# Optimization experiments

Hardware: AMD Instinct MI355X
Metric: run time of the kernel (lower is better)

Reference implementation:

```python
import jax, jax.numpy as jnp
import numpy as np

N, D, E, T, K = 65536, 512, 256, 128, 5
ALPHA = 0.8  # residual_alpha


def _ln(x, gamma, beta, eps=1e-6):
    mu = jnp.mean(x, axis=-1, keepdims=True)
    var = jnp.mean(jnp.square(x - mu), axis=-1, keepdims=True)
    return (x - mu) * jax.lax.rsqrt(var + eps) * gamma + beta


def _normalize(x, eps=1e-6):
    n = jnp.linalg.norm(x, axis=-1, keepdims=True)
    return x / jnp.maximum(n, eps)


def setup_inputs() -> dict:
    key = jax.random.key(0)
    ks = jax.random.split(key, 8)
    return {
        "raw_memory": jax.random.normal(ks[0], (N, D), dtype=jnp.float32),
        "node_features": jax.random.normal(ks[1], (N, E), dtype=jnp.float32),
        "edge_features": jax.random.normal(ks[2], (N, E), dtype=jnp.float32),
        "time_encoding": jax.random.normal(ks[3], (N, T), dtype=jnp.float32),
        "prototypes": jax.random.normal(ks[4], (N, K, D), dtype=jnp.float32),
        "Wq": jax.random.normal(ks[5], (D, D + E + T), dtype=jnp.float32) * 0.02,
        "bq": jnp.zeros((D,), dtype=jnp.float32),
        "Wg": jax.random.normal(ks[6], (1, 2 * D + T), dtype=jnp.float32) * 0.02,
        "bg": jnp.zeros((1,), dtype=jnp.float32),
        "gamma": jnp.ones((D,), dtype=jnp.float32),
        "beta": jnp.zeros((D,), dtype=jnp.float32),
        "temperature": jnp.ones((1,), dtype=jnp.float32),
    }


def reference(raw_memory, node_features, edge_features, time_encoding, prototypes,
              Wq, bq, Wg, bg, gamma, beta, temperature):
    # _sanitize_tensor on finite inputs == clamp (nan_to_num is a no-op)
    raw = jnp.clip(raw_memory, -50.0, 50.0)
    edge_q = jnp.clip(edge_features, -50.0, 50.0)
    time_q = jnp.clip(time_encoding, -50.0, 50.0)

    # query projection (SpectralLinear in eval mode == plain linear) + shared LN + tanh
    q_in = jnp.concatenate([raw, edge_q, time_q], axis=-1)      # [N, D+E+T]
    query = jnp.tanh(_ln(q_in @ Wq.T + bq, gamma, beta))        # [N, D]

    # cosine similarity against per-node prototypes
    q_s = jnp.clip(query, -20.0, 20.0)
    p_s = jnp.clip(prototypes, -20.0, 20.0)
    sim = jnp.einsum('nd,nkd->nk', _normalize(q_s), _normalize(p_s))  # [N, K]
    sim = jnp.clip(sim, -15.0, 15.0)
    temp = jnp.clip(temperature, 0.5, 5.0)
    sim = sim / (temp + 1e-4)

    attn = jnp.clip(jax.nn.softmax(sim, axis=-1), 0.0, 1.0)    # dropout inactive (eval)

    cand = jnp.einsum('nk,nkd->nd', attn, prototypes)           # [N, D]
    cand = jnp.clip(cand, -5.0, 5.0)

    # gate (note: uses raw, un-sanitized time_encoding, then clamps)
    gate_cat = jnp.clip(jnp.concatenate([raw, cand, time_encoding], axis=-1), -30.0, 30.0)
    gate_logits = jnp.clip(gate_cat @ Wg.T + bg, -10.0, 10.0)   # [N, 1]
    g = jax.nn.sigmoid(gate_logits)

    gated = (1.0 - g) * raw + g * cand
    updated = ALPHA * raw + (1.0 - ALPHA) * gated
    updated = jnp.clip(_ln(updated, gamma, beta), -10.0, 10.0)  # final clamp(-50,50) is a no-op
    return updated
```

## Files before the change

kernel.cpp:

```cpp
#include <hip/hip_runtime.h>

#define NROWS 65536
#define DDIM  512
#define EDIM  256
#define TDIM  128
#define KTOT  896
#define MT    32
#define APAD  904

using bf16x8 = __attribute__((ext_vector_type(8))) short;
using f32x4  = __attribute__((ext_vector_type(4))) float;

static __device__ __forceinline__ unsigned short f2bf(float f) {
    unsigned int u = __float_as_uint(f);
    return (unsigned short)((u + 0x7fffu + ((u >> 16) & 1u)) >> 16);
}
static __device__ __forceinline__ float clampf(float x, float lo, float hi) {
    return fminf(fmaxf(x, lo), hi);
}
static __device__ __forceinline__ float wred_sum(float v) {
    #pragma unroll
    for (int m = 32; m > 0; m >>= 1) v += __shfl_xor(v, m, 64);
    return v;
}
static __device__ __forceinline__ float tanh_fast(float x) {
    x = clampf(x, -15.f, 15.f);
    float e = __expf(2.f * x);
    return (e - 1.f) / (e + 1.f);
}

__global__ void k_conv_wq(const float* __restrict__ wq, unsigned short* __restrict__ o) {
    int i = blockIdx.x * 256 + threadIdx.x;
    float4 v = ((const float4*)wq)[i];
    ushort4 r;
    r.x = f2bf(v.x); r.y = f2bf(v.y); r.z = f2bf(v.z); r.w = f2bf(v.w);
    ((ushort4*)o)[i] = r;
}

__global__ __launch_bounds__(256, 2) void k_qproj(
    const float* __restrict__ raw, const float* __restrict__ edge,
    const float* __restrict__ timee, const unsigned short* __restrict__ wqb,
    const float* __restrict__ bq, const float* __restrict__ gamma,
    const float* __restrict__ beta, float* __restrict__ qout)
{
    __shared__ union {
        unsigned short a[MT * APAD];
        float          c[MT * DDIM];
    } sm;

    const int tid = threadIdx.x;
    const int R0  = blockIdx.x * MT;

    #pragma unroll
    for (int i = 0; i < 16; ++i) {
        int idx = i * 256 + tid;
        int row = idx >> 7, c4 = idx & 127;
        float4 v = ((const float4*)(raw + (size_t)(R0 + row) * DDIM))[c4];
        unsigned int lo = (unsigned)f2bf(clampf(v.x, -50.f, 50.f)) |
                          ((unsigned)f2bf(clampf(v.y, -50.f, 50.f)) << 16);
        unsigned int hi = (unsigned)f2bf(clampf(v.z, -50.f, 50.f)) |
                          ((unsigned)f2bf(clampf(v.w, -50.f, 50.f)) << 16);
        *(uint2*)(&sm.a[row * APAD + c4 * 4]) = make_uint2(lo, hi);
    }
    #pragma unroll
    for (int i = 0; i < 8; ++i) {
        int idx = i * 256 + tid;
        int row = idx >> 6, c4 = idx & 63;
        float4 v = ((const float4*)(edge + (size_t)(R0 + row) * EDIM))[c4];
        unsigned int lo = (unsigned)f2bf(clampf(v.x, -50.f, 50.f)) |
                          ((unsigned)f2bf(clampf(v.y, -50.f, 50.f)) << 16);
        unsigned int hi = (unsigned)f2bf(clampf(v.z, -50.f, 50.f)) |
                          ((unsigned)f2bf(clampf(v.w, -50.f, 50.f)) << 16);
        *(uint2*)(&sm.a[row * APAD + DDIM + c4 * 4]) = make_uint2(lo, hi);
    }
    #pragma unroll
    for (int i = 0; i < 4; ++i) {
        int idx = i * 256 + tid;
        int row = idx >> 5, c4 = idx & 31;
        float4 v = ((const float4*)(timee + (size_t)(R0 + row) * TDIM))[c4];
        unsigned int lo = (unsigned)f2bf(clampf(v.x, -50.f, 50.f)) |
                          ((unsigned)f2bf(clampf(v.y, -50.f, 50.f)) << 16);
        unsigned int hi = (unsigned)f2bf(clampf(v.z, -50.f, 50.f)) |
                          ((unsigned)f2bf(clampf(v.w, -50.f, 50.f)) << 16);
        *(uint2*)(&sm.a[row * APAD + DDIM + EDIM + c4 * 4]) = make_uint2(lo, hi);
    }
    __syncthreads();

    const int w = tid >> 6, l = tid & 63, mlo = l & 15, quad = l >> 4;
    f32x4 acc[2][8];
    #pragma unroll
    for (int rt = 0; rt < 2; ++rt)
        #pragma unroll
        for (int c = 0; c < 8; ++c) { acc[rt][c] = (f32x4){0.f, 0.f, 0.f, 0.f}; }

    const unsigned short* bbase  = wqb + (size_t)(w * 128 + mlo) * KTOT + quad * 8;
    const unsigned short* abase0 = &sm.a[ mlo        * APAD + quad * 8];
    const unsigned short* abase1 = &sm.a[(16 + mlo)  * APAD + quad * 8];

    for (int k0 = 0; k0 < KTOT; k0 += 32) {
        bf16x8 a0 = *(const bf16x8*)(abase0 + k0);
        bf16x8 a1 = *(const bf16x8*)(abase1 + k0);
        #pragma unroll
        for (int c = 0; c < 8; ++c) {
            bf16x8 b = *(const bf16x8*)(bbase + (size_t)c * 16 * KTOT + k0);
            acc[0][c] = __builtin_amdgcn_mfma_f32_16x16x32_bf16(a0, b, acc[0][c], 0, 0, 0);
            acc[1][c] = __builtin_amdgcn_mfma_f32_16x16x32_bf16(a1, b, acc[1][c], 0, 0, 0);
        }
    }

    __syncthreads();
    #pragma unroll
    for (int rt = 0; rt < 2; ++rt)
        #pragma unroll
        for (int c = 0; c < 8; ++c)
            #pragma unroll
            for (int r = 0; r < 4; ++r)
                sm.c[(rt * 16 + quad * 4 + r) * DDIM + w * 128 + c * 16 + mlo] = acc[rt][c][r];
    __syncthreads();

    float bqv[8], gv[8], bv[8];
    #pragma unroll
    for (int j = 0; j < 8; ++j) {
        int d = l + 64 * j;
        bqv[j] = bq[d]; gv[j] = gamma[d]; bv[j] = beta[d];
    }
    for (int rr = 0; rr < 8; ++rr) {
        int r = w * 8 + rr;
        float v[8], s = 0.f, sq = 0.f;
        #pragma unroll
        for (int j = 0; j < 8; ++j) {
            v[j] = sm.c[r * DDIM + l + 64 * j] + bqv[j];
            s += v[j]; sq += v[j] * v[j];
        }
        s = wred_sum(s); sq = wred_sum(sq);
        float mu  = s * (1.f / 512.f);
        float var = sq * (1.f / 512.f) - mu * mu;
        float rs  = rsqrtf(fmaxf(var, 0.f) + 1e-6f);
        #pragma unroll
        for (int j = 0; j < 8; ++j) {
            float y = (v[j] - mu) * rs * gv[j] + bv[j];
            qout[(size_t)(R0 + r) * DDIM + l + 64 * j] = tanh_fast(y);
        }
    }
}

__global__ __launch_bounds__(256) void k_attn(
    const float* __restrict__ raw, const float* __restrict__ timee,
    const float* __restrict__ prot, const float* __restrict__ wg,
    const float* __restrict__ bg, const float* __restrict__ gamma,
    const float* __restrict__ beta, const float* __restrict__ temperature,
    float* __restrict__ out)
{
    const int R = blockIdx.x * 4 + (threadIdx.x >> 6);
    const int l = threadIdx.x & 63;
    const size_t rbase = (size_t)R * DDIM;

    float q[8], rw[8], p[5][8], tv[2];
    #pragma unroll
    for (int j = 0; j < 8; ++j) {
        q[j]  = out[rbase + l + 64 * j];
        rw[j] = clampf(raw[rbase + l + 64 * j], -50.f, 50.f);
    }
    tv[0] = timee[(size_t)R * TDIM + l];
    tv[1] = timee[(size_t)R * TDIM + l + 64];
    #pragma unroll
    for (int k = 0; k < 5; ++k)
        #pragma unroll
        for (int j = 0; j < 8; ++j)
            p[k][j] = prot[((size_t)R * 5 + k) * DDIM + l + 64 * j];

    float qs = 0.f;
    #pragma unroll
    for (int j = 0; j < 8; ++j) qs += q[j] * q[j];
    qs = wred_sum(qs);
    float qinv = 1.f / fmaxf(sqrtf(qs), 1e-6f);

    float sim[5];
    #pragma unroll
    for (int k = 0; k < 5; ++k) {
        float d = 0.f, pn = 0.f;
        #pragma unroll
        for (int j = 0; j < 8; ++j) {
            float ps = clampf(p[k][j], -20.f, 20.f);
            d += q[j] * ps; pn += ps * ps;
        }
        d = wred_sum(d); pn = wred_sum(pn);
        sim[k] = d * qinv * (1.f / fmaxf(sqrtf(pn), 1e-6f));
    }
    float temp = clampf(temperature[0], 0.5f, 5.f);
    float tinv = 1.f / (temp + 1e-4f);
    float mx = -1e30f;
    #pragma unroll
    for (int k = 0; k < 5; ++k) { sim[k] = clampf(sim[k], -15.f, 15.f) * tinv; mx = fmaxf(mx, sim[k]); }
    float e[5], Z = 0.f;
    #pragma unroll
    for (int k = 0; k < 5; ++k) { e[k] = __expf(sim[k] - mx); Z += e[k]; }
    float zi = 1.f / Z;
    #pragma unroll
    for (int k = 0; k < 5; ++k) e[k] = clampf(e[k] * zi, 0.f, 1.f);

    float cand[8];
    #pragma unroll
    for (int j = 0; j < 8; ++j) {
        float c = 0.f;
        #pragma unroll
        for (int k = 0; k < 5; ++k) c += e[k] * p[k][j];
        cand[j] = clampf(c, -5.f, 5.f);
    }

    float gp = 0.f;
    #pragma unroll
    for (int j = 0; j < 8; ++j) {
        int d = l + 64 * j;
        gp += wg[d]       * clampf(rw[j],   -30.f, 30.f);
        gp += wg[512 + d] * clampf(cand[j], -30.f, 30.f);
    }
    gp += wg[1024 + l]      * clampf(tv[0], -30.f, 30.f);
    gp += wg[1024 + l + 64] * clampf(tv[1], -30.f, 30.f);
    gp = wred_sum(gp);
    float gl = clampf(gp + bg[0], -10.f, 10.f);
    float g  = 1.f / (1.f + __expf(-gl));

    float u[8], s = 0.f, sq = 0.f;
    #pragma unroll
    for (int j = 0; j < 8; ++j) {
        float gated = (1.f - g) * rw[j] + g * cand[j];
        u[j] = 0.8f * rw[j] + 0.2f * gated;
        s += u[j]; sq += u[j] * u[j];
    }
    s = wred_sum(s); sq = wred_sum(sq);
    float mu  = s * (1.f / 512.f);
    float var = sq * (1.f / 512.f) - mu * mu;
    float rs  = rsqrtf(fmaxf(var, 0.f) + 1e-6f);
    #pragma unroll
    for (int j = 0; j < 8; ++j) {
        int d = l + 64 * j;
        float y = (u[j] - mu) * rs * gamma[d] + beta[d];
        out[rbase + d] = clampf(y, -10.f, 10.f);
    }
}

extern "C" void kernel_launch(void* const* d_in, const int* in_sizes, int n_in,
                              void* d_out, int out_size, void* d_ws, size_t ws_size,
                              hipStream_t stream) {
    const float* raw   = (const float*)d_in[0];
    const float* edge  = (const float*)d_in[2];
    const float* tim   = (const float*)d_in[3];
    const float* prot  = (const float*)d_in[4];
    const float* Wq    = (const float*)d_in[5];
    const float* bq    = (const float*)d_in[6];
    const float* Wg    = (const float*)d_in[7];
    const float* bg    = (const float*)d_in[8];
    const float* gamma = (const float*)d_in[9];
    const float* beta  = (const float*)d_in[10];
    const float* temp  = (const float*)d_in[11];
    float* out = (float*)d_out;
    unsigned short* wqb = (unsigned short*)d_ws;

    k_conv_wq<<<448, 256, 0, stream>>>(Wq, wqb);
    k_qproj<<<NROWS / MT, 256, 0, stream>>>(raw, edge, tim, wqb, bq, gamma, beta, out);
    k_attn <<<NROWS / 4, 256, 0, stream>>>(raw, tim, prot, Wg, bg, gamma, beta, temp, out);
}
```

Baseline: 1.335 ms.

## Fuse query projection with attention/gate epilogue and pre-swizzle Wq into MFMA fragment layout

Merges the query-projection kernel and the prototype attention/gating kernel into one, so the query is consumed from shared memory instead of being written to and re-read from global memory. The bf16 weight conversion now lays Wq out in MFMA B-fragment order, so each lane loads contiguous 16-byte chunks and all eight fragments are issued before the MFMAs. The epilogue switches to float4-vectorized loads and stores. In exchange, each block now does the long per-row attention epilogue serially after the GEMM, with more live registers, which may reduce overlap between the memory-bound and compute phases.

```diff
diff --git a/kernel.cpp b/kernel.cpp
--- a/kernel.cpp
+++ b/kernel.cpp
@@ -1,4 +1,5 @@
 #include <hip/hip_runtime.h>
+
 
 #define NROWS 65536
 #define DDIM  512
@@ -7,6 +8,7 @@
 #define KTOT  896
 #define MT    32
 #define APAD  904
+#define KS    28
 
 using bf16x8 = __attribute__((ext_vector_type(8))) short;
 using f32x4  = __attribute__((ext_vector_type(4))) float;
@@ -30,22 +32,30 @@
 }
 
 __global__ void k_conv_wq(const float* __restrict__ wq, unsigned short* __restrict__ o) {
-    int i = blockIdx.x * 256 + threadIdx.x;
-    float4 v = ((const float4*)wq)[i];
-    ushort4 r;
-    r.x = f2bf(v.x); r.y = f2bf(v.y); r.z = f2bf(v.z); r.w = f2bf(v.w);
-    ((ushort4*)o)[i] = r;
-}
-
-__global__ __launch_bounds__(256, 2) void k_qproj(
+    int t = blockIdx.x * 256 + threadIdx.x;
+    int l = t & 63, rest = t >> 6;
+    int ntile = rest & 31, ks = rest >> 5;
+    const float* src = wq + (size_t)(ntile * 16 + (l & 15)) * KTOT + ks * 32 + (l >> 4) * 8;
+    f32x4 v0 = ((const f32x4*)src)[0];
+    f32x4 v1 = ((const f32x4*)src)[1];
+    union { bf16x8 v; unsigned short u[8]; } r;
+    #pragma unroll
+    for (int j = 0; j < 4; ++j) { r.u[j] = f2bf(v0[j]); r.u[4 + j] = f2bf(v1[j]); }
+    ((bf16x8*)o)[t] = r.v;
+}
+
+__global__ __launch_bounds__(256, 2) void k_fused(
     const float* __restrict__ raw, const float* __restrict__ edge,
-    const float* __restrict__ timee, const unsigned short* __restrict__ wqb,
-    const float* __restrict__ bq, const float* __restrict__ gamma,
-    const float* __restrict__ beta, float* __restrict__ qout)
+    const float* __restrict__ timee, const unsigned short* __restrict__ wqs,
+    const float* __restrict__ bq, const float* __restrict__ wg,
+    const float* __restrict__ bg, const float* __restrict__ gamma,
+    const float* __restrict__ beta, const float* __restrict__ prot,
+    const float* __restrict__ temperature, float* __restrict__ out)
 {
     __shared__ union {
         unsigned short a[MT * APAD];
         float          c[MT * DDIM];
+        f32x4          c4[MT * DDIM / 4];
     } sm;
 
     const int tid = threadIdx.x;
@@ -54,35 +64,35 @@
     #pragma unroll
     for (int i = 0; i < 16; ++i) {
         int idx = i * 256 + tid;
-        int row = idx >> 7, c4 = idx & 127;
-        float4 v = ((const float4*)(raw + (size_t)(R0 + row) * DDIM))[c4];
+        int row = idx >> 7, c4i = idx & 127;
+        float4 v = ((const float4*)(raw + (size_t)(R0 + row) * DDIM))[c4i];
         unsigned int lo = (unsigned)f2bf(clampf(v.x, -50.f, 50.f)) |
                           ((unsigned)f2bf(clampf(v.y, -50.f, 50.f)) << 16);
         unsigned int hi = (unsigned)f2bf(clampf(v.z, -50.f, 50.f)) |
                           ((unsigned)f2bf(clampf(v.w, -50.f, 50.f)) << 16);
-        *(uint2*)(&sm.a[row * APAD + c4 * 4]) = make_uint2(lo, hi);
+        *(uint2*)(&sm.a[row * APAD + c4i * 4]) = make_uint2(lo, hi);
     }
     #pragma unroll
     for (int i = 0; i < 8; ++i) {
         int idx = i * 256 + tid;
-        int row = idx >> 6, c4 = idx & 63;
-        float4 v = ((const float4*)(edge + (size_t)(R0 + row) * EDIM))[c4];
+        int row = idx >> 6, c4i = idx & 63;
+        float4 v = ((const float4*)(edge + (size_t)(R0 + row) * EDIM))[c4i];
         unsigned int lo = (unsigned)f2bf(clampf(v.x, -50.f, 50.f)) |
                           ((unsigned)f2bf(clampf(v.y, -50.f, 50.f)) << 16);
         unsigned int hi = (unsigned)f2bf(clampf(v.z, -50.f, 50.f)) |
                           ((unsigned)f2bf(clampf(v.w, -50.f, 50.f)) << 16);
-        *(uint2*)(&sm.a[row * APAD + DDIM + c4 * 4]) = make_uint2(lo, hi);
+        *(uint2*)(&sm.a[row * APAD + DDIM + c4i * 4]) = make_uint2(lo, hi);
     }
     #pragma unroll
     for (int i = 0; i < 4; ++i) {
         int idx = i * 256 + tid;
-        int row = idx >> 5, c4 = idx & 31;
-        float4 v = ((const float4*)(timee + (size_t)(R0 + row) * TDIM))[c4];
+        int row = idx >> 5, c4i = idx & 31;
+        float4 v = ((const float4*)(timee + (size_t)(R0 + row) * TDIM))[c4i];
         unsigned int lo = (unsigned)f2bf(clampf(v.x, -50.f, 50.f)) |
                           ((unsigned)f2bf(clampf(v.y, -50.f, 50.f)) << 16);
         unsigned int hi = (unsigned)f2bf(clampf(v.z, -50.f, 50.f)) |
                           ((unsigned)f2bf(clampf(v.w, -50.f, 50.f)) << 16);
-        *(uint2*)(&sm.a[row * APAD + DDIM + EDIM + c4 * 4]) = make_uint2(lo, hi);
+        *(uint2*)(&sm.a[row * APAD + DDIM + EDIM + c4i * 4]) = make_uint2(lo, hi);
     }
     __syncthreads();
 
@@ -91,21 +101,24 @@
     #pragma unroll
     for (int rt = 0; rt < 2; ++rt)
         #pragma unroll
-        for (int c = 0; c < 8; ++c) { acc[rt][c] = (f32x4){0.f, 0.f, 0.f, 0.f}; }
-
-    const unsigned short* bbase  = wqb + (size_t)(w * 128 + mlo) * KTOT + quad * 8;
-    const unsigned short* abase0 = &sm.a[ mlo        * APAD + quad * 8];
-    const unsigned short* abase1 = &sm.a[(16 + mlo)  * APAD + quad * 8];
-
-    for (int k0 = 0; k0 < KTOT; k0 += 32) {
-        bf16x8 a0 = *(const bf16x8*)(abase0 + k0);
-        bf16x8 a1 = *(const bf16x8*)(abase1 + k0);
+        for (int c = 0; c < 8; ++c) acc[rt][c] = (f32x4){0.f, 0.f, 0.f, 0.f};
+
+    const unsigned short* abase0 = &sm.a[ mlo       * APAD + quad * 8];
+    const unsigned short* abase1 = &sm.a[(16 + mlo) * APAD + quad * 8];
+    const unsigned short* bptr   = wqs + ((size_t)(w * 8) * 64 + l) * 8;
+
+    for (int ks = 0; ks < KS; ++ks) {
+        bf16x8 a0 = *(const bf16x8*)(abase0 + ks * 32);
+        bf16x8 a1 = *(const bf16x8*)(abase1 + ks * 32);
+        bf16x8 bb[8];
+        #pragma unroll
+        for (int c = 0; c < 8; ++c) bb[c] = *(const bf16x8*)(bptr + c * 512);
         #pragma unroll
         for (int c = 0; c < 8; ++c) {
-            bf16x8 b = *(const bf16x8*)(bbase + (size_t)c * 16 * KTOT + k0);
-            acc[0][c] = __builtin_amdgcn_mfma_f32_16x16x32_bf16(a0, b, acc[0][c], 0, 0, 0);
-            acc[1][c] = __builtin_amdgcn_mfma_f32_16x16x32_bf16(a1, b, acc[1][c], 0, 0, 0);
-        }
+            acc[0][c] = __builtin_amdgcn_mfma_f32_16x16x32_bf16(a0, bb[c], acc[0][c], 0, 0, 0);
+            acc[1][c] = __builtin_amdgcn_mfma_f32_16x16x32_bf16(a1, bb[c], acc[1][c], 0, 0, 0);
+        }
+        bptr += 32 * 64 * 8;
     }
 
     __syncthreads();
@@ -114,129 +127,145 @@
         #pragma unroll
         for (int c = 0; c < 8; ++c)
             #pragma unroll
-            for (int r = 0; r < 4; ++r)
-                sm.c[(rt * 16 + quad * 4 + r) * DDIM + w * 128 + c * 16 + mlo] = acc[rt][c][r];
+            for (int r2 = 0; r2 < 4; ++r2)
+                sm.c[(rt * 16 + quad * 4 + r2) * DDIM + w * 128 + c * 16 + mlo] = acc[rt][c][r2];
     __syncthreads();
 
-    float bqv[8], gv[8], bv[8];
-    #pragma unroll
-    for (int j = 0; j < 8; ++j) {
-        int d = l + 64 * j;
-        bqv[j] = bq[d]; gv[j] = gamma[d]; bv[j] = beta[d];
-    }
+    f32x4 bq4[2], g4[2], b4[2], wgr4[2], wgc4[2];
+    #pragma unroll
+    for (int jj = 0; jj < 2; ++jj) {
+        bq4[jj]  = ((const f32x4*)bq)[l + 64 * jj];
+        g4[jj]   = ((const f32x4*)gamma)[l + 64 * jj];
+        b4[jj]   = ((const f32x4*)beta)[l + 64 * jj];
+        wgr4[jj] = ((const f32x4*)wg)[l + 64 * jj];
+        wgc4[jj] = ((const f32x4*)(wg + DDIM))[l + 64 * jj];
+    }
+    float wgt0 = wg[2 * DDIM + l], wgt1 = wg[2 * DDIM + l + 64];
+    float tmpv = clampf(temperature[0], 0.5f, 5.f);
+    float tinv = 1.f / (tmpv + 1e-4f);
+    float bgv  = bg[0];
+
     for (int rr = 0; rr < 8; ++rr) {
-        int r = w * 8 + rr;
-        float v[8], s = 0.f, sq = 0.f;
-        #pragma unroll
-        for (int j = 0; j < 8; ++j) {
-            v[j] = sm.c[r * DDIM + l + 64 * j] + bqv[j];
-            s += v[j]; sq += v[j] * v[j];
+        const int r = w * 8 + rr;
+        const size_t R = (size_t)(R0 + r);
+        const float* prow = prot + R * (5 * DDIM);
+
+        f32x4 p4[5][2];
+        #pragma unroll
+        for (int k = 0; k < 5; ++k) {
+            p4[k][0] = ((const f32x4*)(prow + k * DDIM))[l];
+            p4[k][1] = ((const f32x4*)(prow + k * DDIM))[l + 64];
+        }
+        f32x4 rw4[2];
+        #pragma unroll
+        for (int jj = 0; jj < 2; ++jj) {
+            f32x4 t = ((const f32x4*)(raw + R * DDIM))[l + 64 * jj];
+            #pragma unroll
+            for (int e2 = 0; e2 < 4; ++e2) rw4[jj][e2] = clampf(t[e2], -50.f, 50.f);
+        }
+        float t0 = timee[R * TDIM + l];
+        float t1 = timee[R * TDIM + l + 64];
+
+        f32x4 v4[2];
+        float s = 0.f, sq = 0.f;
+        #pragma unroll
+        for (int jj = 0; jj < 2; ++jj) {
+            f32x4 cv = sm.c4[r * 128 + l + 64 * jj];
+            cv += bq4[jj];
+            v4[jj] = cv;
+            #pragma unroll
+            for (int e2 = 0; e2 < 4; ++e2) { s += cv[e2]; sq += cv[e2] * cv[e2]; }
         }
         s = wred_sum(s); sq = wred_sum(sq);
         float mu  = s * (1.f / 512.f);
         float var = sq * (1.f / 512.f) - mu * mu;
         float rs  = rsqrtf(fmaxf(var, 0.f) + 1e-6f);
-        #pragma unroll
-        for (int j = 0; j < 8; ++j) {
-            float y = (v[j] - mu) * rs * gv[j] + bv[j];
-            qout[(size_t)(R0 + r) * DDIM + l + 64 * j] = tanh_fast(y);
-        }
-    }
-}
-
-__global__ __launch_bounds__(256) void k_attn(
-    const float* __restrict__ raw, const float* __restrict__ timee,
-    const float* __restrict__ prot, const float* __restrict__ wg,
-    const float* __restrict__ bg, const float* __restrict__ gamma,
-    const float* __restrict__ beta, const float* __restrict__ temperature,
-    float* __restrict__ out)
-{
-    const int R = blockIdx.x * 4 + (threadIdx.x >> 6);
-    const int l = threadIdx.x & 63;
-    const size_t rbase = (size_t)R * DDIM;
-
-    float q[8], rw[8], p[5][8], tv[2];
-    #pragma unroll
-    for (int j = 0; j < 8; ++j) {
-        q[j]  = out[rbase + l + 64 * j];
-        rw[j] = clampf(raw[rbase + l + 64 * j], -50.f, 50.f);
-    }
-    tv[0] = timee[(size_t)R * TDIM + l];
-    tv[1] = timee[(size_t)R * TDIM + l + 64];
-    #pragma unroll
-    for (int k = 0; k < 5; ++k)
-        #pragma unroll
-        for (int j = 0; j < 8; ++j)
-            p[k][j] = prot[((size_t)R * 5 + k) * DDIM + l + 64 * j];
-
-    float qs = 0.f;
-    #pragma unroll
-    for (int j = 0; j < 8; ++j) qs += q[j] * q[j];
-    qs = wred_sum(qs);
-    float qinv = 1.f / fmaxf(sqrtf(qs), 1e-6f);
-
-    float sim[5];
-    #pragma unroll
-    for (int k = 0; k < 5; ++k) {
-        float d = 0.f, pn = 0.f;
-        #pragma unroll
-        for (int j = 0; j < 8; ++j) {
-            float ps = clampf(p[k][j], -20.f, 20.f);
-            d += q[j] * ps; pn += ps * ps;
-        }
-        d = wred_sum(d); pn = wred_sum(pn);
-        sim[k] = d * qinv * (1.f / fmaxf(sqrtf(pn), 1e-6f));
-    }
-    float temp = clampf(temperature[0], 0.5f, 5.f);
-    float tinv = 1.f / (temp + 1e-4f);
-    float mx = -1e30f;
-    #pragma unroll
-    for (int k = 0; k < 5; ++k) { sim[k] = clampf(sim[k], -15.f, 15.f) * tinv; mx = fmaxf(mx, sim[k]); }
-    float e[5], Z = 0.f;
-    #pragma unroll
-    for (int k = 0; k < 5; ++k) { e[k] = __expf(sim[k] - mx); Z += e[k]; }
-    float zi = 1.f / Z;
-    #pragma unroll
-    for (int k = 0; k < 5; ++k) e[k] = clampf(e[k] * zi, 0.f, 1.f);
-
-    float cand[8];
-    #pragma unroll
-    for (int j = 0; j < 8; ++j) {
-        float c = 0.f;
-        #pragma unroll
-        for (int k = 0; k < 5; ++k) c += e[k] * p[k][j];
-        cand[j] = clampf(c, -5.f, 5.f);
-    }
-
-    float gp = 0.f;
-    #pragma unroll
-    for (int j = 0; j < 8; ++j) {
-        int d = l + 64 * j;
-        gp += wg[d]       * clampf(rw[j],   -30.f, 30.f);
-        gp += wg[512 + d] * clampf(cand[j], -30.f, 30.f);
-    }
-    gp += wg[1024 + l]      * clampf(tv[0], -30.f, 30.f);
-    gp += wg[1024 + l + 64] * clampf(tv[1], -30.f, 30.f);
-    gp = wred_sum(gp);
-    float gl = clampf(gp + bg[0], -10.f, 10.f);
-    float g  = 1.f / (1.f + __expf(-gl));
-
-    float u[8], s = 0.f, sq = 0.f;
-    #pragma unroll
-    for (int j = 0; j < 8; ++j) {
-        float gated = (1.f - g) * rw[j] + g * cand[j];
-        u[j] = 0.8f * rw[j] + 0.2f * gated;
-        s += u[j]; sq += u[j] * u[j];
-    }
-    s = wred_sum(s); sq = wred_sum(sq);
-    float mu  = s * (1.f / 512.f);
-    float var = sq * (1.f / 512.f) - mu * mu;
-    float rs  = rsqrtf(fmaxf(var, 0.f) + 1e-6f);
-    #pragma unroll
-    for (int j = 0; j < 8; ++j) {
-        int d = l + 64 * j;
-        float y = (u[j] - mu) * rs * gamma[d] + beta[d];
-        out[rbase + d] = clampf(y, -10.f, 10.f);
+        f32x4 q4[2];
+        float qs = 0.f;
+        #pragma unroll
+        for (int jj = 0; jj < 2; ++jj)
+            #pragma unroll
+            for (int e2 = 0; e2 < 4; ++e2) {
+                float y = (v4[jj][e2] - mu) * rs * g4[jj][e2] + b4[jj][e2];
+                y = tanh_fast(y);
+                q4[jj][e2] = y;
+                qs += y * y;
+            }
+        qs = wred_sum(qs);
+        float qinv = 1.f / fmaxf(sqrtf(qs), 1e-6f);
+
+        float sim[5];
+        #pragma unroll
+        for (int k = 0; k < 5; ++k) {
+            float d = 0.f, pn = 0.f;
+            #pragma unroll
+            for (int jj = 0; jj < 2; ++jj)
+                #pragma unroll
+                for (int e2 = 0; e2 < 4; ++e2) {
+                    float ps = clampf(p4[k][jj][e2], -20.f, 20.f);
+                    d  += q4[jj][e2] * ps;
+                    pn += ps * ps;
+                }
+            d = wred_sum(d); pn = wred_sum(pn);
+            sim[k] = d * qinv * (1.f / fmaxf(sqrtf(pn), 1e-6f));
+        }
+        float mx = -1e30f;
+        #pragma unroll
+        for (int k = 0; k < 5; ++k) { sim[k] = clampf(sim[k], -15.f, 15.f) * tinv; mx = fmaxf(mx, sim[k]); }
+        float ek[5], Z = 0.f;
+        #pragma unroll
+        for (int k = 0; k < 5; ++k) { ek[k] = __expf(sim[k] - mx); Z += ek[k]; }
+        float zi = 1.f / Z;
+        #pragma unroll
+        for (int k = 0; k < 5; ++k) ek[k] = clampf(ek[k] * zi, 0.f, 1.f);
+
+        f32x4 cand4[2];
+        #pragma unroll
+        for (int jj = 0; jj < 2; ++jj) {
+            f32x4 c = (f32x4){0.f, 0.f, 0.f, 0.f};
+            #pragma unroll
+            for (int k = 0; k < 5; ++k) c += ek[k] * p4[k][jj];
+            #pragma unroll
+            for (int e2 = 0; e2 < 4; ++e2) cand4[jj][e2] = clampf(c[e2], -5.f, 5.f);
+        }
+
+        float gp = 0.f;
+        #pragma unroll
+        for (int jj = 0; jj < 2; ++jj)
+            #pragma unroll
+            for (int e2 = 0; e2 < 4; ++e2) {
+                gp += wgr4[jj][e2] * clampf(rw4[jj][e2],   -30.f, 30.f);
+                gp += wgc4[jj][e2] * clampf(cand4[jj][e2], -30.f, 30.f);
+            }
+        gp += wgt0 * clampf(t0, -30.f, 30.f);
+        gp += wgt1 * clampf(t1, -30.f, 30.f);
+        gp = wred_sum(gp);
+        float gl = clampf(gp + bgv, -10.f, 10.f);
+        float g  = 1.f / (1.f + __expf(-gl));
+
+        f32x4 u4[2];
+        s = 0.f; sq = 0.f;
+        #pragma unroll
+        for (int jj = 0; jj < 2; ++jj)
+            #pragma unroll
+            for (int e2 = 0; e2 < 4; ++e2) {
+                float gated = (1.f - g) * rw4[jj][e2] + g * cand4[jj][e2];
+                float u = 0.8f * rw4[jj][e2] + 0.2f * gated;
+                u4[jj][e2] = u;
+                s += u; sq += u * u;
+            }
+        s = wred_sum(s); sq = wred_sum(sq);
+        mu  = s * (1.f / 512.f);
+        var = sq * (1.f / 512.f) - mu * mu;
+        rs  = rsqrtf(fmaxf(var, 0.f) + 1e-6f);
+        #pragma unroll
+        for (int jj = 0; jj < 2; ++jj) {
+            f32x4 y4;
+            #pragma unroll
+            for (int e2 = 0; e2 < 4; ++e2)
+                y4[e2] = clampf((u4[jj][e2] - mu) * rs * g4[jj][e2] + b4[jj][e2], -10.f, 10.f);
+            ((f32x4*)(out + R * DDIM))[l + 64 * jj] = y4;
+        }
     }
 }
 
@@ -257,7 +286,7 @@
     float* out = (float*)d_out;
     unsigned short* wqb = (unsigned short*)d_ws;
 
-    k_conv_wq<<<448, 256, 0, stream>>>(Wq, wqb);
-    k_qproj<<<NROWS / MT, 256, 0, stream>>>(raw, edge, tim, wqb, bq, gamma, beta, out);
-    k_attn <<<NROWS / 4, 256, 0, stream>>>(raw, tim, prot, Wg, bg, gamma, beta, temp, out);
-}
+    k_conv_wq<<<224, 256, 0, stream>>>(Wq, wqb);
+    k_fused<<<NROWS / MT, 256, 0, stream>>>(raw, edge, tim, wqb, bq, Wg, bg,
+                                            gamma, beta, prot, temp, out);
+}
```

Result: faster. 1.182 ms (-11.4%).
